# Performance work log

Measured on AMD Instinct MI355X. Metric: run time of the kernel, lower is better.

## Reference

```python
import jax, jax.numpy as jnp
import numpy as np

B = 1024      # batch
DIN = 103     # generator/encoder input dim
L1, L2 = 64, 32   # encoder layer widths (latent = 32)
E = 8         # NUM_EXPERTS
GH = 64       # gating hidden width
H = 256       # generator hidden width
DOUT = 51     # generator output dim
EPS = 1e-5    # BatchNorm eps


def setup_inputs() -> dict:
    key = jax.random.key(0)
    ks = jax.random.split(key, 24)
    s = 0.05
    f32 = jnp.float32
    return {
        "x": jax.random.normal(ks[0], (B, DIN), f32),
        # encoder Linear + BN params
        "w1": jax.random.normal(ks[1], (L1, DIN), f32) * s,
        "b1": jnp.zeros((L1,), f32),
        "gamma1": jnp.ones((L1,), f32),
        "beta1": jnp.zeros((L1,), f32),
        "w2": jax.random.normal(ks[2], (L2, L1), f32) * s,
        "b2": jnp.zeros((L2,), f32),
        "gamma2": jnp.ones((L2,), f32),
        "beta2": jnp.zeros((L2,), f32),
        # gating MLP (latent 32 -> GH -> GH -> E, ELU, softmax)
        "gw1": jax.random.normal(ks[3], (GH, L2), f32) * s,
        "gb1": jnp.zeros((GH,), f32),
        "gw2": jax.random.normal(ks[4], (GH, GH), f32) * s,
        "gb2": jnp.zeros((GH,), f32),
        "gw3": jax.random.normal(ks[5], (E, GH), f32) * s,
        "gb3": jnp.zeros((E,), f32),
        # expert weight banks for 3-layer generator (MANN style)
        "ew1": jax.random.normal(ks[6], (E, DIN, H), f32) * s,
        "eb1": jnp.zeros((E, H), f32),
        "ew2": jax.random.normal(ks[7], (E, H, H), f32) * s,
        "eb2": jnp.zeros((E, H), f32),
        "ew3": jax.random.normal(ks[8], (E, H, DOUT), f32) * s,
        "eb3": jnp.zeros((E, DOUT), f32),
    }


def _batchnorm(h, gamma, beta):
    # training-mode BatchNorm1d: per-batch mean/var (biased var, matching torch)
    m = jnp.mean(h, axis=0)
    v = jnp.mean((h - m) ** 2, axis=0)
    return gamma * (h - m) * jax.lax.rsqrt(v + EPS) + beta


def reference(x, w1, b1, gamma1, beta1, w2, b2, gamma2, beta2,
              gw1, gb1, gw2, gb2, gw3, gb3,
              ew1, eb1, ew2, eb2, ew3, eb3):
    # in-place scale of last 3 features (x[:,100:103] *= 100)
    xs = x.at[:, 100:103].multiply(100.0)
    # encoder: Linear -> BN -> ReLU, twice
    h = jax.nn.relu(_batchnorm(xs @ w1.T + b1, gamma1, beta1))
    latent = jax.nn.relu(_batchnorm(h @ w2.T + b2, gamma2, beta2))
    # gating network -> blending coefficients BC [B, E]
    g = jax.nn.elu(latent @ gw1.T + gb1)
    g = jax.nn.elu(g @ gw2.T + gb2)
    bc = jax.nn.softmax(g @ gw3.T + gb3, axis=-1)
    # MANN-style generator: per-sample expert-blended weights
    wb1 = jnp.einsum('be,eih->bih', bc, ew1)   # [B, DIN, H]
    h1 = jax.nn.elu(jnp.einsum('bi,bih->bh', xs, wb1) + bc @ eb1)
    wb2 = jnp.einsum('be,ehk->bhk', bc, ew2)   # [B, H, H]
    h2 = jax.nn.elu(jnp.einsum('bh,bhk->bk', h1, wb2) + bc @ eb2)
    wb3 = jnp.einsum('be,eho->bho', bc, ew3)   # [B, H, DOUT]
    out = jnp.einsum('bh,bho->bo', h2, wb3) + bc @ eb3
    return out
```

## Files before the change

### kernel.cpp

```cpp
#include <hip/hip_runtime.h>
#include <math.h>


#define DIN 103
#define NE  8
#define HH  256
#define DOUT 51
#define EPSBN 1e-5f

typedef __attribute__((ext_vector_type(8))) short bf16x8;
typedef __attribute__((ext_vector_type(4))) float f32x4;
typedef __attribute__((ext_vector_type(8))) unsigned short us8;
typedef unsigned short ushort_t;

__device__ __forceinline__ float eluf(float v) { return v > 0.f ? v : (expf(v) - 1.f); }
__device__ __forceinline__ unsigned short bf16h(float f) {
  unsigned u = __float_as_uint(f);
  u += 0x7FFFu + ((u >> 16) & 1u);
  return (unsigned short)(u >> 16);
}
__device__ __forceinline__ float bf16f(unsigned short h) { return __uint_as_float(((unsigned)h) << 16); }
__device__ __forceinline__ void split_bf16(float v, unsigned short& h, unsigned short& l) {
  h = bf16h(v);
  l = bf16h(v - bf16f(h));
}
#define MFMA __builtin_amdgcn_mfma_f32_16x16x32_bf16

#define O_SLOTS1 0
#define O_SLOTS2 8192
#define O_BCG    12288
#define O_H1RAW  20480
#define O_H2RAW  86016
#define O_XSH    118784
#define O_XSL    184320
#define O_W1H    249856
#define O_W1L    253952
#define O_E1H    258048
#define O_E1L    389120
#define O_E2H    520192
#define O_E2L    782336
#define O_E3H    1044480
#define O_E3L    1110016
#define O_A1H    1175552
#define O_A1L    1306624
#define O_A2H    1437696
#define O_A2L    1568768
#define O_P      1699840

__global__ __launch_bounds__(256) void k_prep(
    const float* __restrict__ x, const float* __restrict__ w1,
    const float* __restrict__ ew1, const float* __restrict__ ew2, const float* __restrict__ ew3,
    float* __restrict__ ws) {
  __shared__ float tile[32][65];
  int bk = blockIdx.x, t = threadIdx.x;
  int l2 = t & 63, c = l2 & 15, q = l2 >> 4;

  if (bk < 256) {
    int nh = bk & 3, kc = (bk >> 2) & 7, e = bk >> 5;
    int k0 = kc * 32, n0 = nh * 64;
#pragma unroll
    for (int i = 0; i < 8; ++i) {
      int kl = (t >> 6) + i * 4;
      tile[kl][t & 63] = ew2[((size_t)e * HH + k0 + kl) * HH + n0 + (t & 63)];
    }
    __syncthreads();
    int nsl = t >> 6;
    us8 H8, L8;
#pragma unroll
    for (int j = 0; j < 8; ++j) {
      unsigned short h, lo; split_bf16(tile[q * 8 + j][nsl * 16 + c], h, lo);
      H8[j] = h; L8[j] = lo;
    }
    size_t dst = (((size_t)(e * 16 + nh * 4 + nsl)) * 8 + kc) * 512 + l2 * 8;
    *(us8*)((ushort_t*)(ws + O_E2H) + dst) = H8;
    *(us8*)((ushort_t*)(ws + O_E2L) + dst) = L8;
  } else if (bk < 384) {
    int b2 = bk - 256;
    int nh = b2 & 3, kc = (b2 >> 2) & 3, e = b2 >> 4;
    int k0 = kc * 32, n0 = nh * 64;
#pragma unroll
    for (int i = 0; i < 8; ++i) {
      int kl = (t >> 6) + i * 4;
      int k = k0 + kl;
      tile[kl][t & 63] = (k < DIN) ? ew1[((size_t)e * DIN + k) * HH + n0 + (t & 63)] : 0.f;
    }
    __syncthreads();
    int nsl = t >> 6;
    us8 H8, L8;
#pragma unroll
    for (int j = 0; j < 8; ++j) {
      unsigned short h, lo; split_bf16(tile[q * 8 + j][nsl * 16 + c], h, lo);
      H8[j] = h; L8[j] = lo;
    }
    size_t dst = (((size_t)(e * 16 + nh * 4 + nsl)) * 4 + kc) * 512 + l2 * 8;
    *(us8*)((ushort_t*)(ws + O_E1H) + dst) = H8;
    *(us8*)((ushort_t*)(ws + O_E1L) + dst) = L8;
  } else if (bk < 448) {
    int b2 = bk - 384;
    int kc = b2 & 7, e = b2 >> 3;
    int k0 = kc * 32;
#pragma unroll
    for (int i = 0; i < 8; ++i) {
      int kl = (t >> 6) + i * 4;
      int n = t & 63;
      tile[kl][n] = (n < DOUT) ? ew3[((size_t)e * HH + k0 + kl) * DOUT + n] : 0.f;
    }
    __syncthreads();
    int nsl = t >> 6;
    us8 H8, L8;
#pragma unroll
    for (int j = 0; j < 8; ++j) {
      unsigned short h, lo; split_bf16(tile[q * 8 + j][nsl * 16 + c], h, lo);
      H8[j] = h; L8[j] = lo;
    }
    size_t dst = (((size_t)(e * 4 + nsl)) * 8 + kc) * 512 + l2 * 8;
    *(us8*)((ushort_t*)(ws + O_E3H) + dst) = H8;
    *(us8*)((ushort_t*)(ws + O_E3L) + dst) = L8;
  } else if (bk < 452) {
    int kc = bk - 448;
    int k0 = kc * 32;
    __shared__ float tw[64][33];
#pragma unroll
    for (int p8 = 0; p8 < 8; ++p8) {
      int j = (t >> 5) + p8 * 8;
      int kl = t & 31;
      int k = k0 + kl;
      tw[j][kl] = (k < DIN) ? w1[(size_t)j * DIN + k] : 0.f;
    }
    __syncthreads();
    int nsl = t >> 6;
    us8 H8, L8;
#pragma unroll
    for (int j = 0; j < 8; ++j) {
      unsigned short h, lo; split_bf16(tw[nsl * 16 + c][q * 8 + j], h, lo);
      H8[j] = h; L8[j] = lo;
    }
    size_t dst = ((size_t)nsl * 4 + kc) * 512 + l2 * 8;
    *(us8*)((ushort_t*)(ws + O_W1H) + dst) = H8;
    *(us8*)((ushort_t*)(ws + O_W1L) + dst) = L8;
  } else {
    int msub = bk - 452;
    __shared__ float xt[16][104];
    for (int i = t; i < 16 * 104; i += 256) {
      int b = i / 104, k = i - b * 104;
      float v = 0.f;
      if (k < DIN) { v = x[(size_t)(msub * 16 + b) * DIN + k]; if (k >= 100) v *= 100.f; }
      xt[b][k] = v;
    }
    __syncthreads();
    int kc = t >> 6;
    int m = c;
    us8 H8, L8;
#pragma unroll
    for (int j = 0; j < 8; ++j) {
      int k = kc * 32 + q * 8 + j;
      float v = (k < 104) ? xt[m][k] : 0.f;
      unsigned short h, lo; split_bf16(v, h, lo);
      H8[j] = h; L8[j] = lo;
    }
    size_t dst = ((size_t)msub * 4 + kc) * 512 + l2 * 8;
    *(us8*)((ushort_t*)(ws + O_XSH) + dst) = H8;
    *(us8*)((ushort_t*)(ws + O_XSL) + dst) = L8;
  }
}

__global__ __launch_bounds__(256) void k_enc1(const float* __restrict__ b1, float* __restrict__ ws) {
  __shared__ float tile[16][65];
  int bk = blockIdx.x, t = threadIdx.x;
  int wv = t >> 6, l = t & 63, c = l & 15, quad = l >> 4;
  const ushort_t* XsH = (const ushort_t*)(ws + O_XSH);
  const ushort_t* XsL = (const ushort_t*)(ws + O_XSL);
  const ushort_t* W1H = (const ushort_t*)(ws + O_W1H);
  const ushort_t* W1L = (const ushort_t*)(ws + O_W1L);
  float* h1raw  = ws + O_H1RAW;
  float* slots1 = ws + O_SLOTS1;
  f32x4 acc = {0.f, 0.f, 0.f, 0.f};
#pragma unroll
  for (int kc = 0; kc < 4; ++kc) {
    bf16x8 ah = *(const bf16x8*)(XsH + ((size_t)bk * 4 + kc) * 512 + l * 8);
    bf16x8 al = *(const bf16x8*)(XsL + ((size_t)bk * 4 + kc) * 512 + l * 8);
    bf16x8 bh = *(const bf16x8*)(W1H + ((size_t)wv * 4 + kc) * 512 + l * 8);
    bf16x8 bl = *(const bf16x8*)(W1L + ((size_t)wv * 4 + kc) * 512 + l * 8);
    acc = MFMA(ah, bh, acc, 0, 0, 0);
    acc = MFMA(al, bh, acc, 0, 0, 0);
    acc = MFMA(ah, bl, acc, 0, 0, 0);
  }
  int col = wv * 16 + c;
  float b1v = b1[col];
#pragma unroll
  for (int r = 0; r < 4; ++r) {
    float v = acc[r] + b1v;
    tile[quad * 4 + r][col] = v;
    h1raw[(size_t)(bk * 16 + quad * 4 + r) * 64 + col] = v;
  }
  __syncthreads();
  if (t < 64) {
    float s = 0.f, qq = 0.f;
    for (int r = 0; r < 16; ++r) { float v = tile[r][t]; s += v; qq += v * v; }
    slots1[bk * 128 + t] = s;
    slots1[bk * 128 + 64 + t] = qq;
  }
}

__global__ __launch_bounds__(256) void k_enc2(
    const float* __restrict__ gamma1, const float* __restrict__ beta1,
    const float* __restrict__ w2, const float* __restrict__ b2, float* __restrict__ ws) {
  __shared__ float w2T[64 * 33];
  __shared__ float red[128];
  __shared__ float sc1[64], sh1[64];
  __shared__ float h1b[16][64];
  __shared__ float hb2[16][32];
  float* slots1 = ws + O_SLOTS1;
  float* slots2 = ws + O_SLOTS2;
  float* h1raw  = ws + O_H1RAW;
  float* h2raw  = ws + O_H2RAW;
  int bk = blockIdx.x, t = threadIdx.x;
  int R0 = bk * 16;
  for (int i = t; i < 2048; i += 256) { int j = i >> 6, k = i & 63; w2T[k * 33 + j] = w2[i]; }
  if (t < 128) {
    float s = 0.f;
    for (int b = 0; b < 64; ++b) s += slots1[b * 128 + t];
    red[t] = s;
  }
  __syncthreads();
  if (t < 64) {
    float m = red[t] * (1.f / 1024.f);
    float v = red[64 + t] * (1.f / 1024.f) - m * m;
    float sc = gamma1[t] * rsqrtf(v + EPSBN);
    sc1[t] = sc; sh1[t] = beta1[t] - m * sc;
  }
  __syncthreads();
#pragma unroll
  for (int i = 0; i < 4; ++i) {
    int idx = t + i * 256;
    int r = idx >> 6, k = idx & 63;
    h1b[r][k] = fmaxf(fmaf(h1raw[(size_t)(R0 + r) * 64 + k], sc1[k], sh1[k]), 0.f);
  }
  __syncthreads();
#pragma unroll
  for (int i = 0; i < 2; ++i) {
    int o = t + i * 256;
    int r = o >> 5, j = o & 31;
    float acc = b2[j];
    for (int k = 0; k < 64; ++k) acc = fmaf(h1b[r][k], w2T[k * 33 + j], acc);
    hb2[r][j] = acc;
    h2raw[(size_t)(R0 + r) * 32 + j] = acc;
  }
  __syncthreads();
  if (t < 32) {
    float s = 0.f, q = 0.f;
    for (int r = 0; r < 16; ++r) { float v = hb2[r][t]; s += v; q += v * v; }
    slots2[bk * 64 + t] = s;
    slots2[bk * 64 + 32 + t] = q;
  }
}

__global__ __launch_bounds__(256) void k_gate(
    const float* __restrict__ gamma2, const float* __restrict__ beta2,
    const float* __restrict__ gw1, const float* __restrict__ gb1,
    const float* __restrict__ gw2, const float* __restrict__ gb2,
    const float* __restrict__ gw3, const float* __restrict__ gb3,
    float* __restrict__ ws) {
  __shared__ float red2[64], sc2[32], sh2[32];
  __shared__ float lat[16][32];
  __shared__ float gw1L[64 * 33], gw2L[64 * 65], gw3L[8 * 65];
  __shared__ float gb1L[64], gb2L[64], gb3L[8];
  __shared__ float g1[16][64], g2[16][64];
  float* slots2 = ws + O_SLOTS2;
  float* bcg    = ws + O_BCG;
  float* h2raw  = ws + O_H2RAW;
  int bk = blockIdx.x, t = threadIdx.x;
  int wv = t >> 6, l = t & 63;
  int R0 = bk * 16;
  for (int i = t; i < 2048; i += 256) { int j = i >> 5, k = i & 31; gw1L[j * 33 + k] = gw1[i]; }
  for (int i = t; i < 4096; i += 256) { int j = i >> 6, k = i & 63; gw2L[j * 65 + k] = gw2[i]; }
  for (int i = t; i < 512; i += 256) { int j = i >> 6, k = i & 63; gw3L[j * 65 + k] = gw3[i]; }
  if (t < 64) { gb1L[t] = gb1[t]; gb2L[t] = gb2[t]; }
  if (t < 8) gb3L[t] = gb3[t];
  if (t < 64) {
    float s = 0.f;
    for (int b = 0; b < 64; ++b) s += slots2[b * 64 + t];
    red2[t] = s;
  }
  __syncthreads();
  if (t < 32) {
    float m = red2[t] * (1.f / 1024.f);
    float v = red2[32 + t] * (1.f / 1024.f) - m * m;
    float sc = gamma2[t] * rsqrtf(v + EPSBN);
    sc2[t] = sc; sh2[t] = beta2[t] - m * sc;
  }
  __syncthreads();
#pragma unroll
  for (int i = 0; i < 2; ++i) {
    int idx = t + i * 256;
    int r = idx >> 5, cc = idx & 31;
    lat[r][cc] = fmaxf(fmaf(h2raw[(size_t)(R0 + r) * 32 + cc], sc2[cc], sh2[cc]), 0.f);
  }
  __syncthreads();
#pragma unroll
  for (int rr = 0; rr < 4; ++rr) {
    int r = wv * 4 + rr;
    float a1 = gb1L[l];
    for (int k = 0; k < 32; ++k) a1 = fmaf(gw1L[l * 33 + k], lat[r][k], a1);
    g1[r][l] = eluf(a1);
  }
  __syncthreads();
#pragma unroll
  for (int rr = 0; rr < 4; ++rr) {
    int r = wv * 4 + rr;
    float a2 = gb2L[l];
    for (int k = 0; k < 64; ++k) a2 = fmaf(gw2L[l * 65 + k], g1[r][k], a2);
    g2[r][l] = eluf(a2);
  }
  __syncthreads();
#pragma unroll
  for (int rr = 0; rr < 4; ++rr) {
    int r = wv * 4 + rr;
    if (l < 8) {
      float a3 = gb3L[l];
      for (int k = 0; k < 64; ++k) a3 = fmaf(gw3L[l * 65 + k], g2[r][k], a3);
      float mx = a3;
      mx = fmaxf(mx, __shfl_xor(mx, 1));
      mx = fmaxf(mx, __shfl_xor(mx, 2));
      mx = fmaxf(mx, __shfl_xor(mx, 4));
      float p = expf(a3 - mx);
      float sp = p;
      sp += __shfl_xor(sp, 1); sp += __shfl_xor(sp, 2); sp += __shfl_xor(sp, 4);
      bcg[(size_t)(R0 + r) * 8 + l] = p / sp;
    }
  }
}

__global__ __launch_bounds__(256) void k_gen1(float* __restrict__ ws) {
  int bk = blockIdx.x, e = blockIdx.y, t = threadIdx.x;
  int wv = t >> 6, l = t & 63, c = l & 15, quad = l >> 4;
  const ushort_t* XsH = (const ushort_t*)(ws + O_XSH);
  const ushort_t* XsL = (const ushort_t*)(ws + O_XSL);
  const ushort_t* E1H = (const ushort_t*)(ws + O_E1H);
  const ushort_t* E1L = (const ushort_t*)(ws + O_E1L);
  float* p = ws + O_P;
  f32x4 acc[4] = {};
#pragma unroll
  for (int kc = 0; kc < 4; ++kc) {
    bf16x8 ah = *(const bf16x8*)(XsH + ((size_t)bk * 4 + kc) * 512 + l * 8);
    bf16x8 al = *(const bf16x8*)(XsL + ((size_t)bk * 4 + kc) * 512 + l * 8);
#pragma unroll
    for (int nsi = 0; nsi < 4; ++nsi) {
      int ns = wv * 4 + nsi;
      size_t bo = (((size_t)(e * 16 + ns)) * 4 + kc) * 512 + l * 8;
      bf16x8 bh = *(const bf16x8*)(E1H + bo);
      bf16x8 bl = *(const bf16x8*)(E1L + bo);
      acc[nsi] = MFMA(ah, bh, acc[nsi], 0, 0, 0);
      acc[nsi] = MFMA(al, bh, acc[nsi], 0, 0, 0);
      acc[nsi] = MFMA(ah, bl, acc[nsi], 0, 0, 0);
    }
  }
  float* pe = p + (size_t)e * 262144;
#pragma unroll
  for (int nsi = 0; nsi < 4; ++nsi) {
    int col = (wv * 4 + nsi) * 16 + c;
#pragma unroll
    for (int r = 0; r < 4; ++r)
      pe[(size_t)(bk * 16 + quad * 4 + r) * 256 + col] = acc[nsi][r];
  }
}

__global__ __launch_bounds__(256) void k_gen2(float* __restrict__ ws) {
  int bk = blockIdx.x, e = blockIdx.y, t = threadIdx.x;
  int wv = t >> 6, l = t & 63, c = l & 15, quad = l >> 4;
  const ushort_t* AH = (const ushort_t*)(ws + O_A1H);
  const ushort_t* AL = (const ushort_t*)(ws + O_A1L);
  const ushort_t* E2H = (const ushort_t*)(ws + O_E2H);
  const ushort_t* E2L = (const ushort_t*)(ws + O_E2L);
  float* p = ws + O_P;
  f32x4 acc[4] = {};
#pragma unroll
  for (int kc = 0; kc < 8; ++kc) {
    bf16x8 ah = *(const bf16x8*)(AH + ((size_t)bk * 8 + kc) * 512 + l * 8);
    bf16x8 al = *(const bf16x8*)(AL + ((size_t)bk * 8 + kc) * 512 + l * 8);
#pragma unroll
    for (int nsi = 0; nsi < 4; ++nsi) {
      int ns = wv * 4 + nsi;
      size_t bo = (((size_t)(e * 16 + ns)) * 8 + kc) * 512 + l * 8;
      bf16x8 bh = *(const bf16x8*)(E2H + bo);
      bf16x8 bl = *(const bf16x8*)(E2L + bo);
      acc[nsi] = MFMA(ah, bh, acc[nsi], 0, 0, 0);
      acc[nsi] = MFMA(al, bh, acc[nsi], 0, 0, 0);
      acc[nsi] = MFMA(ah, bl, acc[nsi], 0, 0, 0);
    }
  }
  float* pe = p + (size_t)e * 262144;
#pragma unroll
  for (int nsi = 0; nsi < 4; ++nsi) {
    int col = (wv * 4 + nsi) * 16 + c;
#pragma unroll
    for (int r = 0; r < 4; ++r)
      pe[(size_t)(bk * 16 + quad * 4 + r) * 256 + col] = acc[nsi][r];
  }
}

__global__ __launch_bounds__(256) void k_gen3(float* __restrict__ ws) {
  int bk = blockIdx.x, eg = blockIdx.y, t = threadIdx.x;
  int wv = t >> 6, l = t & 63, c = l & 15, quad = l >> 4;
  int e = eg * 4 + wv;
  const ushort_t* AH = (const ushort_t*)(ws + O_A2H);
  const ushort_t* AL = (const ushort_t*)(ws + O_A2L);
  const ushort_t* E3H = (const ushort_t*)(ws + O_E3H);
  const ushort_t* E3L = (const ushort_t*)(ws + O_E3L);
  float* p3 = ws + O_P;
  f32x4 acc[4] = {};
#pragma unroll
  for (int kc = 0; kc < 8; ++kc) {
    bf16x8 ah = *(const bf16x8*)(AH + ((size_t)bk * 8 + kc) * 512 + l * 8);
    bf16x8 al = *(const bf16x8*)(AL + ((size_t)bk * 8 + kc) * 512 + l * 8);
#pragma unroll
    for (int nsi = 0; nsi < 4; ++nsi) {
      size_t bo = (((size_t)(e * 4 + nsi)) * 8 + kc) * 512 + l * 8;
      bf16x8 bh = *(const bf16x8*)(E3H + bo);
      bf16x8 bl = *(const bf16x8*)(E3L + bo);
      acc[nsi] = MFMA(ah, bh, acc[nsi], 0, 0, 0);
      acc[nsi] = MFMA(al, bh, acc[nsi], 0, 0, 0);
      acc[nsi] = MFMA(ah, bl, acc[nsi], 0, 0, 0);
    }
  }
  float* pe = p3 + (size_t)e * 65536;
#pragma unroll
  for (int nsi = 0; nsi < 4; ++nsi) {
    int col = nsi * 16 + c;
#pragma unroll
    for (int r = 0; r < 4; ++r)
      pe[(size_t)(bk * 16 + quad * 4 + r) * 64 + col] = acc[nsi][r];
  }
}

__global__ __launch_bounds__(256) void k_comb(const float* __restrict__ eb,
    float* __restrict__ ws, int dstH, int dstL) {
  int gid = blockIdx.x * 256 + threadIdx.x;
  int l2 = gid & 63, kc = (gid >> 6) & 7, msub = gid >> 9;
  int b = msub * 16 + (l2 & 15);
  int k0 = kc * 32 + (l2 >> 4) * 8;
  const float* p = ws + O_P;
  const float* bc = ws + O_BCG;
  unsigned short* ah = (unsigned short*)(ws + dstH);
  unsigned short* al = (unsigned short*)(ws + dstL);
  float wv[NE];
#pragma unroll
  for (int e = 0; e < NE; ++e) wv[e] = bc[b * NE + e];
  float s[8] = {};
#pragma unroll
  for (int e = 0; e < NE; ++e) {
    const float* pr = p + (size_t)e * 262144 + (size_t)b * HH + k0;
    float4 p0 = *(const float4*)pr, p1 = *(const float4*)(pr + 4);
    const float* er = eb + e * HH + k0;
    float4 e0 = *(const float4*)er, e1 = *(const float4*)(er + 4);
    s[0] = fmaf(wv[e], p0.x + e0.x, s[0]);
    s[1] = fmaf(wv[e], p0.y + e0.y, s[1]);
    s[2] = fmaf(wv[e], p0.z + e0.z, s[2]);
    s[3] = fmaf(wv[e], p0.w + e0.w, s[3]);
    s[4] = fmaf(wv[e], p1.x + e1.x, s[4]);
    s[5] = fmaf(wv[e], p1.y + e1.y, s[5]);
    s[6] = fmaf(wv[e], p1.z + e1.z, s[6]);
    s[7] = fmaf(wv[e], p1.w + e1.w, s[7]);
  }
  us8 H, L;
#pragma unroll
  for (int j = 0; j < 8; ++j) {
    float v = eluf(s[j]);
    unsigned short h, lo; split_bf16(v, h, lo);
    H[j] = h; L[j] = lo;
  }
  *(us8*)(ah + (size_t)gid * 8) = H;
  *(us8*)(al + (size_t)gid * 8) = L;
}

__global__ __launch_bounds__(256) void k_comb3(const float* __restrict__ eb3,
    float* __restrict__ ws, float* __restrict__ out) {
  int gid = blockIdx.x * 256 + threadIdx.x;
  int b = gid >> 6, o = gid & 63;
  if (o >= DOUT) return;
  const float* p3 = ws + O_P;
  const float* bc = ws + O_BCG;
  float s = 0.f;
#pragma unroll
  for (int e = 0; e < NE; ++e)
    s = fmaf(bc[b * NE + e], p3[(size_t)e * 65536 + (size_t)b * 64 + o] + eb3[e * DOUT + o], s);
  out[(size_t)b * DOUT + o] = s;
}

extern "C" void kernel_launch(void* const* d_in, const int* in_sizes, int n_in,
                              void* d_out, int out_size, void* d_ws, size_t ws_size,
                              hipStream_t stream) {
  const float* x      = (const float*)d_in[0];
  const float* w1     = (const float*)d_in[1];
  const float* b1     = (const float*)d_in[2];
  const float* gamma1 = (const float*)d_in[3];
  const float* beta1  = (const float*)d_in[4];
  const float* w2     = (const float*)d_in[5];
  const float* b2     = (const float*)d_in[6];
  const float* gamma2 = (const float*)d_in[7];
  const float* beta2  = (const float*)d_in[8];
  const float* gw1    = (const float*)d_in[9];
  const float* gb1    = (const float*)d_in[10];
  const float* gw2    = (const float*)d_in[11];
  const float* gb2    = (const float*)d_in[12];
  const float* gw3    = (const float*)d_in[13];
  const float* gb3    = (const float*)d_in[14];
  const float* ew1    = (const float*)d_in[15];
  const float* eb1    = (const float*)d_in[16];
  const float* ew2    = (const float*)d_in[17];
  const float* eb2    = (const float*)d_in[18];
  const float* ew3    = (const float*)d_in[19];
  const float* eb3    = (const float*)d_in[20];
  float* wsf  = (float*)d_ws;
  float* outp = (float*)d_out;

  k_prep<<<516, 256, 0, stream>>>(x, w1, ew1, ew2, ew3, wsf);
  k_enc1<<<64, 256, 0, stream>>>(b1, wsf);
  k_enc2<<<64, 256, 0, stream>>>(gamma1, beta1, w2, b2, wsf);
  k_gate<<<64, 256, 0, stream>>>(gamma2, beta2, gw1, gb1, gw2, gb2, gw3, gb3, wsf);
  k_gen1<<<dim3(64, 8), 256, 0, stream>>>(wsf);
  k_comb<<<128, 256, 0, stream>>>(eb1, wsf, O_A1H, O_A1L);
  k_gen2<<<dim3(64, 8), 256, 0, stream>>>(wsf);
  k_comb<<<128, 256, 0, stream>>>(eb2, wsf, O_A2H, O_A2L);
  k_gen3<<<dim3(64, 2), 256, 0, stream>>>(wsf);
  k_comb3<<<256, 256, 0, stream>>>(eb3, wsf, outp);
}
```

Measured before the change: 166.7 us.

## Fuse prep/enc1, gen1/gate, and expert-combine steps into gen kernels

Cuts the launch chain from ten kernels to five. Encoder layer 1 now runs as a scalar FMA matmul inside the prep kernel, and gen1 runs concurrently with the gating network in one grid. Each expert-combine step (blend + bias + ELU + bf16 split) is recomputed inside the next generator kernel through shared memory instead of a separate pass, and the final blend is done in registers in gen3. The intent is to remove launch gaps and intermediate round trips to global memory. In exchange, gen2c redoes the combine for each of the 8 experts, and gen2 and gen3 each read all 8 expert outputs.

Result: slower. 186.1 us (+11.7%).

```diff
diff --git a/kernel.cpp b/kernel.cpp
--- a/kernel.cpp
+++ b/kernel.cpp
@@ -33,25 +33,23 @@
 #define O_H2RAW  86016
 #define O_XSH    118784
 #define O_XSL    184320
-#define O_W1H    249856
-#define O_W1L    253952
-#define O_E1H    258048
-#define O_E1L    389120
-#define O_E2H    520192
-#define O_E2L    782336
-#define O_E3H    1044480
-#define O_E3L    1110016
-#define O_A1H    1175552
-#define O_A1L    1306624
-#define O_A2H    1437696
-#define O_A2L    1568768
-#define O_P      1699840
-
-__global__ __launch_bounds__(256) void k_prep(
-    const float* __restrict__ x, const float* __restrict__ w1,
+#define O_E1H    249856
+#define O_E1L    380928
+#define O_E2H    512000
+#define O_E2L    774144
+#define O_E3H    1036288
+#define O_E3L    1101824
+#define O_P      1167360
+#define O_P2     3264512
+
+__global__ __launch_bounds__(256) void k_prep_enc1(
+    const float* __restrict__ x, const float* __restrict__ w1, const float* __restrict__ b1,
     const float* __restrict__ ew1, const float* __restrict__ ew2, const float* __restrict__ ew3,
     float* __restrict__ ws) {
   __shared__ float tile[32][65];
+  __shared__ float w1L[64 * DIN];
+  __shared__ float xr16[16][104];
+  __shared__ float hb[16][64];
   int bk = blockIdx.x, t = threadIdx.x;
   int l2 = t & 63, c = l2 & 15, q = l2 >> 4;
 
@@ -116,89 +114,56 @@
     size_t dst = (((size_t)(e * 4 + nsl)) * 8 + kc) * 512 + l2 * 8;
     *(us8*)((ushort_t*)(ws + O_E3H) + dst) = H8;
     *(us8*)((ushort_t*)(ws + O_E3L) + dst) = L8;
-  } else if (bk < 452) {
-    int kc = bk - 448;
-    int k0 = kc * 32;
-    __shared__ float tw[64][33];
-#pragma unroll
-    for (int p8 = 0; p8 < 8; ++p8) {
-      int j = (t >> 5) + p8 * 8;
-      int kl = t & 31;
-      int k = k0 + kl;
-      tw[j][kl] = (k < DIN) ? w1[(size_t)j * DIN + k] : 0.f;
-    }
-    __syncthreads();
-    int nsl = t >> 6;
-    us8 H8, L8;
-#pragma unroll
-    for (int j = 0; j < 8; ++j) {
-      unsigned short h, lo; split_bf16(tw[nsl * 16 + c][q * 8 + j], h, lo);
-      H8[j] = h; L8[j] = lo;
-    }
-    size_t dst = ((size_t)nsl * 4 + kc) * 512 + l2 * 8;
-    *(us8*)((ushort_t*)(ws + O_W1H) + dst) = H8;
-    *(us8*)((ushort_t*)(ws + O_W1L) + dst) = L8;
-  } else {
-    int msub = bk - 452;
-    __shared__ float xt[16][104];
+  } else if (bk < 512) {
+    int msub = bk - 448;
     for (int i = t; i < 16 * 104; i += 256) {
       int b = i / 104, k = i - b * 104;
       float v = 0.f;
       if (k < DIN) { v = x[(size_t)(msub * 16 + b) * DIN + k]; if (k >= 100) v *= 100.f; }
-      xt[b][k] = v;
+      xr16[b][k] = v;
     }
     __syncthreads();
     int kc = t >> 6;
-    int m = c;
     us8 H8, L8;
 #pragma unroll
     for (int j = 0; j < 8; ++j) {
       int k = kc * 32 + q * 8 + j;
-      float v = (k < 104) ? xt[m][k] : 0.f;
+      float v = (k < 104) ? xr16[c][k] : 0.f;
       unsigned short h, lo; split_bf16(v, h, lo);
       H8[j] = h; L8[j] = lo;
     }
     size_t dst = ((size_t)msub * 4 + kc) * 512 + l2 * 8;
     *(us8*)((ushort_t*)(ws + O_XSH) + dst) = H8;
     *(us8*)((ushort_t*)(ws + O_XSL) + dst) = L8;
-  }
-}
-
-__global__ __launch_bounds__(256) void k_enc1(const float* __restrict__ b1, float* __restrict__ ws) {
-  __shared__ float tile[16][65];
-  int bk = blockIdx.x, t = threadIdx.x;
-  int wv = t >> 6, l = t & 63, c = l & 15, quad = l >> 4;
-  const ushort_t* XsH = (const ushort_t*)(ws + O_XSH);
-  const ushort_t* XsL = (const ushort_t*)(ws + O_XSL);
-  const ushort_t* W1H = (const ushort_t*)(ws + O_W1H);
-  const ushort_t* W1L = (const ushort_t*)(ws + O_W1L);
-  float* h1raw  = ws + O_H1RAW;
-  float* slots1 = ws + O_SLOTS1;
-  f32x4 acc = {0.f, 0.f, 0.f, 0.f};
-#pragma unroll
-  for (int kc = 0; kc < 4; ++kc) {
-    bf16x8 ah = *(const bf16x8*)(XsH + ((size_t)bk * 4 + kc) * 512 + l * 8);
-    bf16x8 al = *(const bf16x8*)(XsL + ((size_t)bk * 4 + kc) * 512 + l * 8);
-    bf16x8 bh = *(const bf16x8*)(W1H + ((size_t)wv * 4 + kc) * 512 + l * 8);
-    bf16x8 bl = *(const bf16x8*)(W1L + ((size_t)wv * 4 + kc) * 512 + l * 8);
-    acc = MFMA(ah, bh, acc, 0, 0, 0);
-    acc = MFMA(al, bh, acc, 0, 0, 0);
-    acc = MFMA(ah, bl, acc, 0, 0, 0);
-  }
-  int col = wv * 16 + c;
-  float b1v = b1[col];
-#pragma unroll
-  for (int r = 0; r < 4; ++r) {
-    float v = acc[r] + b1v;
-    tile[quad * 4 + r][col] = v;
-    h1raw[(size_t)(bk * 16 + quad * 4 + r) * 64 + col] = v;
-  }
-  __syncthreads();
-  if (t < 64) {
-    float s = 0.f, qq = 0.f;
-    for (int r = 0; r < 16; ++r) { float v = tile[r][t]; s += v; qq += v * v; }
-    slots1[bk * 128 + t] = s;
-    slots1[bk * 128 + 64 + t] = qq;
+  } else {
+    float* slots1 = ws + O_SLOTS1;
+    float* h1raw  = ws + O_H1RAW;
+    int bkl = bk - 512;
+    int r0 = bkl * 16;
+    for (int i = t; i < 64 * DIN; i += 256) w1L[i] = w1[i];
+    for (int i = t; i < 16 * 104; i += 256) {
+      int r = i / 104, c2 = i - r * 104;
+      float v = 0.f;
+      if (c2 < DIN) { v = x[(size_t)(r0 + r) * DIN + c2]; if (c2 >= 100) v *= 100.f; }
+      xr16[r][c2] = v;
+    }
+    __syncthreads();
+#pragma unroll
+    for (int i = 0; i < 4; ++i) {
+      int idx = t + i * 256;
+      int r = idx >> 6, j = idx & 63;
+      float acc = b1[j];
+      for (int k = 0; k < DIN; ++k) acc = fmaf(xr16[r][k], w1L[j * DIN + k], acc);
+      hb[r][j] = acc;
+      h1raw[(size_t)(r0 + r) * 64 + j] = acc;
+    }
+    __syncthreads();
+    if (t < 64) {
+      float s = 0.f, qq = 0.f;
+      for (int r = 0; r < 16; ++r) { float v = hb[r][t]; s += v; qq += v * v; }
+      slots1[bkl * 128 + t] = s;
+      slots1[bkl * 128 + 64 + t] = qq;
+    }
   }
 }
 
@@ -255,141 +220,182 @@
   }
 }
 
-__global__ __launch_bounds__(256) void k_gate(
+__global__ __launch_bounds__(256) void k_gen1_gate(
     const float* __restrict__ gamma2, const float* __restrict__ beta2,
     const float* __restrict__ gw1, const float* __restrict__ gb1,
     const float* __restrict__ gw2, const float* __restrict__ gb2,
     const float* __restrict__ gw3, const float* __restrict__ gb3,
     float* __restrict__ ws) {
-  __shared__ float red2[64], sc2[32], sh2[32];
-  __shared__ float lat[16][32];
-  __shared__ float gw1L[64 * 33], gw2L[64 * 65], gw3L[8 * 65];
-  __shared__ float gb1L[64], gb2L[64], gb3L[8];
-  __shared__ float g1[16][64], g2[16][64];
-  float* slots2 = ws + O_SLOTS2;
-  float* bcg    = ws + O_BCG;
-  float* h2raw  = ws + O_H2RAW;
-  int bk = blockIdx.x, t = threadIdx.x;
+  int blk = blockIdx.x, t = threadIdx.x;
   int wv = t >> 6, l = t & 63;
+  if (blk < 512) {
+    int bk = blk >> 3, e = blk & 7;
+    int c = l & 15, quad = l >> 4;
+    const ushort_t* XsH = (const ushort_t*)(ws + O_XSH);
+    const ushort_t* XsL = (const ushort_t*)(ws + O_XSL);
+    const ushort_t* E1H = (const ushort_t*)(ws + O_E1H);
+    const ushort_t* E1L = (const ushort_t*)(ws + O_E1L);
+    float* p = ws + O_P;
+    f32x4 acc[4] = {};
+#pragma unroll
+    for (int kc = 0; kc < 4; ++kc) {
+      bf16x8 ah = *(const bf16x8*)(XsH + ((size_t)bk * 4 + kc) * 512 + l * 8);
+      bf16x8 al = *(const bf16x8*)(XsL + ((size_t)bk * 4 + kc) * 512 + l * 8);
+#pragma unroll
+      for (int nsi = 0; nsi < 4; ++nsi) {
+        int ns = wv * 4 + nsi;
+        size_t bo = (((size_t)(e * 16 + ns)) * 4 + kc) * 512 + l * 8;
+        bf16x8 bh = *(const bf16x8*)(E1H + bo);
+        bf16x8 bl = *(const bf16x8*)(E1L + bo);
+        acc[nsi] = MFMA(ah, bh, acc[nsi], 0, 0, 0);
+        acc[nsi] = MFMA(al, bh, acc[nsi], 0, 0, 0);
+        acc[nsi] = MFMA(ah, bl, acc[nsi], 0, 0, 0);
+      }
+    }
+    float* pe = p + (size_t)e * 262144;
+#pragma unroll
+    for (int nsi = 0; nsi < 4; ++nsi) {
+      int col = (wv * 4 + nsi) * 16 + c;
+#pragma unroll
+      for (int r = 0; r < 4; ++r)
+        pe[(size_t)(bk * 16 + quad * 4 + r) * 256 + col] = acc[nsi][r];
+    }
+  } else {
+    __shared__ float red2[64], sc2[32], sh2[32];
+    __shared__ float lat[16][32];
+    __shared__ float gw1L[64 * 33], gw2L[64 * 65], gw3L[8 * 65];
+    __shared__ float gb1L[64], gb2L[64], gb3L[8];
+    __shared__ float g1[16][64], g2[16][64];
+    float* slots2 = ws + O_SLOTS2;
+    float* bcg    = ws + O_BCG;
+    float* h2raw  = ws + O_H2RAW;
+    int bk = blk - 512;
+    int R0 = bk * 16;
+    for (int i = t; i < 2048; i += 256) { int j = i >> 5, k = i & 31; gw1L[j * 33 + k] = gw1[i]; }
+    for (int i = t; i < 4096; i += 256) { int j = i >> 6, k = i & 63; gw2L[j * 65 + k] = gw2[i]; }
+    for (int i = t; i < 512; i += 256) { int j = i >> 6, k = i & 63; gw3L[j * 65 + k] = gw3[i]; }
+    if (t < 64) { gb1L[t] = gb1[t]; gb2L[t] = gb2[t]; }
+    if (t < 8) gb3L[t] = gb3[t];
+    if (t < 64) {
+      float s = 0.f;
+      for (int b = 0; b < 64; ++b) s += slots2[b * 64 + t];
+      red2[t] = s;
+    }
+    __syncthreads();
+    if (t < 32) {
+      float m = red2[t] * (1.f / 1024.f);
+      float v = red2[32 + t] * (1.f / 1024.f) - m * m;
+      float sc = gamma2[t] * rsqrtf(v + EPSBN);
+      sc2[t] = sc; sh2[t] = beta2[t] - m * sc;
+    }
+    __syncthreads();
+#pragma unroll
+    for (int i = 0; i < 2; ++i) {
+      int idx = t + i * 256;
+      int r = idx >> 5, cc = idx & 31;
+      lat[r][cc] = fmaxf(fmaf(h2raw[(size_t)(R0 + r) * 32 + cc], sc2[cc], sh2[cc]), 0.f);
+    }
+    __syncthreads();
+#pragma unroll
+    for (int rr = 0; rr < 4; ++rr) {
+      int r = wv * 4 + rr;
+      float a1 = gb1L[l];
+      for (int k = 0; k < 32; ++k) a1 = fmaf(gw1L[l * 33 + k], lat[r][k], a1);
+      g1[r][l] = eluf(a1);
+    }
+    __syncthreads();
+#pragma unroll
+    for (int rr = 0; rr < 4; ++rr) {
+      int r = wv * 4 + rr;
+      float a2 = gb2L[l];
+      for (int k = 0; k < 64; ++k) a2 = fmaf(gw2L[l * 65 + k], g1[r][k], a2);
+      g2[r][l] = eluf(a2);
+    }
+    __syncthreads();
+#pragma unroll
+    for (int rr = 0; rr < 4; ++rr) {
+      int r = wv * 4 + rr;
+      if (l < 8) {
+        float a3 = gb3L[l];
+        for (int k = 0; k < 64; ++k) a3 = fmaf(gw3L[l * 65 + k], g2[r][k], a3);
+        float mx = a3;
+        mx = fmaxf(mx, __shfl_xor(mx, 1));
+        mx = fmaxf(mx, __shfl_xor(mx, 2));
+        mx = fmaxf(mx, __shfl_xor(mx, 4));
+        float p = expf(a3 - mx);
+        float sp = p;
+        sp += __shfl_xor(sp, 1); sp += __shfl_xor(sp, 2); sp += __shfl_xor(sp, 4);
+        bcg[(size_t)(R0 + r) * 8 + l] = p / sp;
+      }
+    }
+  }
+}
+
+__global__ __launch_bounds__(256) void k_gen2c(const float* __restrict__ eb1, float* __restrict__ ws) {
+  __shared__ __attribute__((aligned(16))) unsigned short aHs[4096], aLs[4096];
+  int bk = blockIdx.x, e = blockIdx.y, t = threadIdx.x;
+  int wv = t >> 6, l = t & 63, c = l & 15, quad = l >> 4;
   int R0 = bk * 16;
-  for (int i = t; i < 2048; i += 256) { int j = i >> 5, k = i & 31; gw1L[j * 33 + k] = gw1[i]; }
-  for (int i = t; i < 4096; i += 256) { int j = i >> 6, k = i & 63; gw2L[j * 65 + k] = gw2[i]; }
-  for (int i = t; i < 512; i += 256) { int j = i >> 6, k = i & 63; gw3L[j * 65 + k] = gw3[i]; }
-  if (t < 64) { gb1L[t] = gb1[t]; gb2L[t] = gb2[t]; }
-  if (t < 8) gb3L[t] = gb3[t];
-  if (t < 64) {
-    float s = 0.f;
-    for (int b = 0; b < 64; ++b) s += slots2[b * 64 + t];
-    red2[t] = s;
-  }
-  __syncthreads();
-  if (t < 32) {
-    float m = red2[t] * (1.f / 1024.f);
-    float v = red2[32 + t] * (1.f / 1024.f) - m * m;
-    float sc = gamma2[t] * rsqrtf(v + EPSBN);
-    sc2[t] = sc; sh2[t] = beta2[t] - m * sc;
-  }
-  __syncthreads();
+  const float* P   = ws + O_P;
+  const float* bcg = ws + O_BCG;
+  const ushort_t* E2H = (const ushort_t*)(ws + O_E2H);
+  const ushort_t* E2L = (const ushort_t*)(ws + O_E2L);
+  float* P2 = ws + O_P2;
 #pragma unroll
   for (int i = 0; i < 2; ++i) {
     int idx = t + i * 256;
-    int r = idx >> 5, cc = idx & 31;
-    lat[r][cc] = fmaxf(fmaf(h2raw[(size_t)(R0 + r) * 32 + cc], sc2[cc], sh2[cc]), 0.f);
-  }
-  __syncthreads();
-#pragma unroll
-  for (int rr = 0; rr < 4; ++rr) {
-    int r = wv * 4 + rr;
-    float a1 = gb1L[l];
-    for (int k = 0; k < 32; ++k) a1 = fmaf(gw1L[l * 33 + k], lat[r][k], a1);
-    g1[r][l] = eluf(a1);
-  }
-  __syncthreads();
-#pragma unroll
-  for (int rr = 0; rr < 4; ++rr) {
-    int r = wv * 4 + rr;
-    float a2 = gb2L[l];
-    for (int k = 0; k < 64; ++k) a2 = fmaf(gw2L[l * 65 + k], g1[r][k], a2);
-    g2[r][l] = eluf(a2);
-  }
-  __syncthreads();
-#pragma unroll
-  for (int rr = 0; rr < 4; ++rr) {
-    int r = wv * 4 + rr;
-    if (l < 8) {
-      float a3 = gb3L[l];
-      for (int k = 0; k < 64; ++k) a3 = fmaf(gw3L[l * 65 + k], g2[r][k], a3);
-      float mx = a3;
-      mx = fmaxf(mx, __shfl_xor(mx, 1));
-      mx = fmaxf(mx, __shfl_xor(mx, 2));
-      mx = fmaxf(mx, __shfl_xor(mx, 4));
-      float p = expf(a3 - mx);
-      float sp = p;
-      sp += __shfl_xor(sp, 1); sp += __shfl_xor(sp, 2); sp += __shfl_xor(sp, 4);
-      bcg[(size_t)(R0 + r) * 8 + l] = p / sp;
-    }
-  }
-}
-
-__global__ __launch_bounds__(256) void k_gen1(float* __restrict__ ws) {
-  int bk = blockIdx.x, e = blockIdx.y, t = threadIdx.x;
-  int wv = t >> 6, l = t & 63, c = l & 15, quad = l >> 4;
-  const ushort_t* XsH = (const ushort_t*)(ws + O_XSH);
-  const ushort_t* XsL = (const ushort_t*)(ws + O_XSL);
-  const ushort_t* E1H = (const ushort_t*)(ws + O_E1H);
-  const ushort_t* E1L = (const ushort_t*)(ws + O_E1L);
-  float* p = ws + O_P;
+    int kc = idx >> 6, l2 = idx & 63;
+    int b = R0 + (l2 & 15);
+    int k0 = kc * 32 + (l2 >> 4) * 8;
+    float s[8] = {};
+#pragma unroll
+    for (int e2 = 0; e2 < 8; ++e2) {
+      float w8 = bcg[b * 8 + e2];
+      const float* pr = P + (size_t)e2 * 262144 + (size_t)b * 256 + k0;
+      float4 p0 = *(const float4*)pr, p1 = *(const float4*)(pr + 4);
+      const float* er = eb1 + e2 * 256 + k0;
+      float4 e0 = *(const float4*)er, e1 = *(const float4*)(er + 4);
+      s[0] = fmaf(w8, p0.x + e0.x, s[0]);
+      s[1] = fmaf(w8, p0.y + e0.y, s[1]);
+      s[2] = fmaf(w8, p0.z + e0.z, s[2]);
+      s[3] = fmaf(w8, p0.w + e0.w, s[3]);
+      s[4] = fmaf(w8, p1.x + e1.x, s[4]);
+      s[5] = fmaf(w8, p1.y + e1.y, s[5]);
+      s[6] = fmaf(w8, p1.z + e1.z, s[6]);
+      s[7] = fmaf(w8, p1.w + e1.w, s[7]);
+    }
+    us8 H, L;
+#pragma unroll
+    for (int j = 0; j < 8; ++j) {
+      float v = eluf(s[j]);
+      unsigned short h, lo; split_bf16(v, h, lo);
+      H[j] = h; L[j] = lo;
+    }
+    *(us8*)(aHs + idx * 8) = H;
+    *(us8*)(aLs + idx * 8) = L;
+  }
+  __syncthreads();
+  bf16x8 ah[8], al[8];
+#pragma unroll
+  for (int kc = 0; kc < 8; ++kc) {
+    ah[kc] = *(const bf16x8*)(aHs + kc * 512 + l * 8);
+    al[kc] = *(const bf16x8*)(aLs + kc * 512 + l * 8);
+  }
   f32x4 acc[4] = {};
 #pragma unroll
-  for (int kc = 0; kc < 4; ++kc) {
-    bf16x8 ah = *(const bf16x8*)(XsH + ((size_t)bk * 4 + kc) * 512 + l * 8);
-    bf16x8 al = *(const bf16x8*)(XsL + ((size_t)bk * 4 + kc) * 512 + l * 8);
-#pragma unroll
-    for (int nsi = 0; nsi < 4; ++nsi) {
-      int ns = wv * 4 + nsi;
-      size_t bo = (((size_t)(e * 16 + ns)) * 4 + kc) * 512 + l * 8;
-      bf16x8 bh = *(const bf16x8*)(E1H + bo);
-      bf16x8 bl = *(const bf16x8*)(E1L + bo);
-      acc[nsi] = MFMA(ah, bh, acc[nsi], 0, 0, 0);
-      acc[nsi] = MFMA(al, bh, acc[nsi], 0, 0, 0);
-      acc[nsi] = MFMA(ah, bl, acc[nsi], 0, 0, 0);
-    }
-  }
-  float* pe = p + (size_t)e * 262144;
-#pragma unroll
-  for (int nsi = 0; nsi < 4; ++nsi) {
-    int col = (wv * 4 + nsi) * 16 + c;
-#pragma unroll
-    for (int r = 0; r < 4; ++r)
-      pe[(size_t)(bk * 16 + quad * 4 + r) * 256 + col] = acc[nsi][r];
-  }
-}
-
-__global__ __launch_bounds__(256) void k_gen2(float* __restrict__ ws) {
-  int bk = blockIdx.x, e = blockIdx.y, t = threadIdx.x;
-  int wv = t >> 6, l = t & 63, c = l & 15, quad = l >> 4;
-  const ushort_t* AH = (const ushort_t*)(ws + O_A1H);
-  const ushort_t* AL = (const ushort_t*)(ws + O_A1L);
-  const ushort_t* E2H = (const ushort_t*)(ws + O_E2H);
-  const ushort_t* E2L = (const ushort_t*)(ws + O_E2L);
-  float* p = ws + O_P;
-  f32x4 acc[4] = {};
-#pragma unroll
   for (int kc = 0; kc < 8; ++kc) {
-    bf16x8 ah = *(const bf16x8*)(AH + ((size_t)bk * 8 + kc) * 512 + l * 8);
-    bf16x8 al = *(const bf16x8*)(AL + ((size_t)bk * 8 + kc) * 512 + l * 8);
 #pragma unroll
     for (int nsi = 0; nsi < 4; ++nsi) {
       int ns = wv * 4 + nsi;
       size_t bo = (((size_t)(e * 16 + ns)) * 8 + kc) * 512 + l * 8;
       bf16x8 bh = *(const bf16x8*)(E2H + bo);
       bf16x8 bl = *(const bf16x8*)(E2L + bo);
-      acc[nsi] = MFMA(ah, bh, acc[nsi], 0, 0, 0);
-      acc[nsi] = MFMA(al, bh, acc[nsi], 0, 0, 0);
-      acc[nsi] = MFMA(ah, bl, acc[nsi], 0, 0, 0);
-    }
-  }
-  float* pe = p + (size_t)e * 262144;
+      acc[nsi] = MFMA(ah[kc], bh, acc[nsi], 0, 0, 0);
+      acc[nsi] = MFMA(al[kc], bh, acc[nsi], 0, 0, 0);
+      acc[nsi] = MFMA(ah[kc], bl, acc[nsi], 0, 0, 0);
+    }
+  }
+  float* pe = P2 + (size_t)e * 262144;
 #pragma unroll
   for (int nsi = 0; nsi < 4; ++nsi) {
     int col = (wv * 4 + nsi) * 16 + c;
@@ -399,92 +405,101 @@
   }
 }
 
-__global__ __launch_bounds__(256) void k_gen3(float* __restrict__ ws) {
-  int bk = blockIdx.x, eg = blockIdx.y, t = threadIdx.x;
+__global__ __launch_bounds__(256) void k_gen3c(const float* __restrict__ eb2,
+    const float* __restrict__ eb3, float* __restrict__ ws, float* __restrict__ out) {
+  __shared__ __attribute__((aligned(16))) unsigned short aHs[4096], aLs[4096];
+  __shared__ float bcL[16][8];
+  __shared__ float eb3L[8][64];
+  __shared__ float p3s[4][16][64];
+  int bk = blockIdx.x, t = threadIdx.x;
   int wv = t >> 6, l = t & 63, c = l & 15, quad = l >> 4;
-  int e = eg * 4 + wv;
-  const ushort_t* AH = (const ushort_t*)(ws + O_A2H);
-  const ushort_t* AL = (const ushort_t*)(ws + O_A2L);
+  int R0 = bk * 16;
+  const float* P2  = ws + O_P2;
+  const float* bcg = ws + O_BCG;
   const ushort_t* E3H = (const ushort_t*)(ws + O_E3H);
   const ushort_t* E3L = (const ushort_t*)(ws + O_E3L);
-  float* p3 = ws + O_P;
-  f32x4 acc[4] = {};
+  if (t < 128) bcL[t >> 3][t & 7] = bcg[(size_t)(R0 + (t >> 3)) * 8 + (t & 7)];
+  for (int i = t; i < 512; i += 256) {
+    int e = i >> 6, n = i & 63;
+    eb3L[e][n] = (n < DOUT) ? eb3[e * DOUT + n] : 0.f;
+  }
+#pragma unroll
+  for (int i = 0; i < 2; ++i) {
+    int idx = t + i * 256;
+    int kc = idx >> 6, l2 = idx & 63;
+    int b = R0 + (l2 & 15);
+    int k0 = kc * 32 + (l2 >> 4) * 8;
+    float s[8] = {};
+#pragma unroll
+    for (int e2 = 0; e2 < 8; ++e2) {
+      float w8 = bcg[b * 8 + e2];
+      const float* pr = P2 + (size_t)e2 * 262144 + (size_t)b * 256 + k0;
+      float4 p0 = *(const float4*)pr, p1 = *(const float4*)(pr + 4);
+      const float* er = eb2 + e2 * 256 + k0;
+      float4 e0 = *(const float4*)er, e1 = *(const float4*)(er + 4);
+      s[0] = fmaf(w8, p0.x + e0.x, s[0]);
+      s[1] = fmaf(w8, p0.y + e0.y, s[1]);
+      s[2] = fmaf(w8, p0.z + e0.z, s[2]);
+      s[3] = fmaf(w8, p0.w + e0.w, s[3]);
+      s[4] = fmaf(w8, p1.x + e1.x, s[4]);
+      s[5] = fmaf(w8, p1.y + e1.y, s[5]);
+      s[6] = fmaf(w8, p1.z + e1.z, s[6]);
+      s[7] = fmaf(w8, p1.w + e1.w, s[7]);
+    }
+    us8 H, L;
+#pragma unroll
+    for (int j = 0; j < 8; ++j) {
+      float v = eluf(s[j]);
+      unsigned short h, lo; split_bf16(v, h, lo);
+      H[j] = h; L[j] = lo;
+    }
+    *(us8*)(aHs + idx * 8) = H;
+    *(us8*)(aLs + idx * 8) = L;
+  }
+  __syncthreads();
+  bf16x8 ah[8], al[8];
 #pragma unroll
   for (int kc = 0; kc < 8; ++kc) {
-    bf16x8 ah = *(const bf16x8*)(AH + ((size_t)bk * 8 + kc) * 512 + l * 8);
-    bf16x8 al = *(const bf16x8*)(AL + ((size_t)bk * 8 + kc) * 512 + l * 8);
+    ah[kc] = *(const bf16x8*)(aHs + kc * 512 + l * 8);
+    al[kc] = *(const bf16x8*)(aLs + kc * 512 + l * 8);
+  }
+  f32x4 tot[4] = {};
+#pragma unroll
+  for (int ei = 0; ei < 2; ++ei) {
+    int e = wv * 2 + ei;
 #pragma unroll
     for (int nsi = 0; nsi < 4; ++nsi) {
-      size_t bo = (((size_t)(e * 4 + nsi)) * 8 + kc) * 512 + l * 8;
-      bf16x8 bh = *(const bf16x8*)(E3H + bo);
-      bf16x8 bl = *(const bf16x8*)(E3L + bo);
-      acc[nsi] = MFMA(ah, bh, acc[nsi], 0, 0, 0);
-      acc[nsi] = MFMA(al, bh, acc[nsi], 0, 0, 0);
-      acc[nsi] = MFMA(ah, bl, acc[nsi], 0, 0, 0);
-    }
-  }
-  float* pe = p3 + (size_t)e * 65536;
-#pragma unroll
-  for (int nsi = 0; nsi < 4; ++nsi) {
-    int col = nsi * 16 + c;
+      f32x4 acc = {0.f, 0.f, 0.f, 0.f};
+#pragma unroll
+      for (int kc = 0; kc < 8; ++kc) {
+        size_t bo = (((size_t)(e * 4 + nsi)) * 8 + kc) * 512 + l * 8;
+        bf16x8 bh = *(const bf16x8*)(E3H + bo);
+        bf16x8 bl = *(const bf16x8*)(E3L + bo);
+        acc = MFMA(ah[kc], bh, acc, 0, 0, 0);
+        acc = MFMA(al[kc], bh, acc, 0, 0, 0);
+        acc = MFMA(ah[kc], bl, acc, 0, 0, 0);
+      }
+#pragma unroll
+      for (int r = 0; r < 4; ++r)
+        tot[nsi][r] = fmaf(bcL[quad * 4 + r][e], acc[r], tot[nsi][r]);
+    }
+  }
+#pragma unroll
+  for (int nsi = 0; nsi < 4; ++nsi)
 #pragma unroll
     for (int r = 0; r < 4; ++r)
-      pe[(size_t)(bk * 16 + quad * 4 + r) * 64 + col] = acc[nsi][r];
-  }
-}
-
-__global__ __launch_bounds__(256) void k_comb(const float* __restrict__ eb,
-    float* __restrict__ ws, int dstH, int dstL) {
-  int gid = blockIdx.x * 256 + threadIdx.x;
-  int l2 = gid & 63, kc = (gid >> 6) & 7, msub = gid >> 9;
-  int b = msub * 16 + (l2 & 15);
-  int k0 = kc * 32 + (l2 >> 4) * 8;
-  const float* p = ws + O_P;
-  const float* bc = ws + O_BCG;
-  unsigned short* ah = (unsigned short*)(ws + dstH);
-  unsigned short* al = (unsigned short*)(ws + dstL);
-  float wv[NE];
-#pragma unroll
-  for (int e = 0; e < NE; ++e) wv[e] = bc[b * NE + e];
-  float s[8] = {};
-#pragma unroll
-  for (int e = 0; e < NE; ++e) {
-    const float* pr = p + (size_t)e * 262144 + (size_t)b * HH + k0;
-    float4 p0 = *(const float4*)pr, p1 = *(const float4*)(pr + 4);
-    const float* er = eb + e * HH + k0;
-    float4 e0 = *(const float4*)er, e1 = *(const float4*)(er + 4);
-    s[0] = fmaf(wv[e], p0.x + e0.x, s[0]);
-    s[1] = fmaf(wv[e], p0.y + e0.y, s[1]);
-    s[2] = fmaf(wv[e], p0.z + e0.z, s[2]);
-    s[3] = fmaf(wv[e], p0.w + e0.w, s[3]);
-    s[4] = fmaf(wv[e], p1.x + e1.x, s[4]);
-    s[5] = fmaf(wv[e], p1.y + e1.y, s[5]);
-    s[6] = fmaf(wv[e], p1.z + e1.z, s[6]);
-    s[7] = fmaf(wv[e], p1.w + e1.w, s[7]);
-  }
-  us8 H, L;
-#pragma unroll
-  for (int j = 0; j < 8; ++j) {
-    float v = eluf(s[j]);
-    unsigned short h, lo; split_bf16(v, h, lo);
-    H[j] = h; L[j] = lo;
-  }
-  *(us8*)(ah + (size_t)gid * 8) = H;
-  *(us8*)(al + (size_t)gid * 8) = L;
-}
-
-__global__ __launch_bounds__(256) void k_comb3(const float* __restrict__ eb3,
-    float* __restrict__ ws, float* __restrict__ out) {
-  int gid = blockIdx.x * 256 + threadIdx.x;
-  int b = gid >> 6, o = gid & 63;
-  if (o >= DOUT) return;
-  const float* p3 = ws + O_P;
-  const float* bc = ws + O_BCG;
-  float s = 0.f;
-#pragma unroll
-  for (int e = 0; e < NE; ++e)
-    s = fmaf(bc[b * NE + e], p3[(size_t)e * 65536 + (size_t)b * 64 + o] + eb3[e * DOUT + o], s);
-  out[(size_t)b * DOUT + o] = s;
+      p3s[wv][quad * 4 + r][nsi * 16 + c] = tot[nsi][r];
+  __syncthreads();
+#pragma unroll
+  for (int i = 0; i < 4; ++i) {
+    int idx = t + i * 256;
+    int row = idx >> 6, col = idx & 63;
+    float s = p3s[0][row][col] + p3s[1][row][col] + p3s[2][row][col] + p3s[3][row][col];
+    float bb = 0.f;
+#pragma unroll
+    for (int e = 0; e < 8; ++e) bb = fmaf(bcL[row][e], eb3L[e][col], bb);
+    if (col < DOUT) out[(size_t)(R0 + row) * DOUT + col] = s + bb;
+  }
 }
 
 extern "C" void kernel_launch(void* const* d_in, const int* in_sizes, int n_in,
@@ -514,14 +529,9 @@
   float* wsf  = (float*)d_ws;
   float* outp = (float*)d_out;
 
-  k_prep<<<516, 256, 0, stream>>>(x, w1, ew1, ew2, ew3, wsf);
-  k_enc1<<<64, 256, 0, stream>>>(b1, wsf);
+  k_prep_enc1<<<576, 256, 0, stream>>>(x, w1, b1, ew1, ew2, ew3, wsf);
   k_enc2<<<64, 256, 0, stream>>>(gamma1, beta1, w2, b2, wsf);
-  k_gate<<<64, 256, 0, stream>>>(gamma2, beta2, gw1, gb1, gw2, gb2, gw3, gb3, wsf);
-  k_gen1<<<dim3(64, 8), 256, 0, stream>>>(wsf);
-  k_comb<<<128, 256, 0, stream>>>(eb1, wsf, O_A1H, O_A1L);
-  k_gen2<<<dim3(64, 8), 256, 0, stream>>>(wsf);
-  k_comb<<<128, 256, 0, stream>>>(eb2, wsf, O_A2H, O_A2L);
-  k_gen3<<<dim3(64, 2), 256, 0, stream>>>(wsf);
-  k_comb3<<<256, 256, 0, stream>>>(eb3, wsf, outp);
-}
+  k_gen1_gate<<<576, 256, 0, stream>>>(gamma2, beta2, gw1, gb1, gw2, gb2, gw3, gb3, wsf);
+  k_gen2c<<<dim3(64, 8), 256, 0, stream>>>(eb1, wsf);
+  k_gen3c<<<64, 256, 0, stream>>>(eb2, eb3, wsf, outp);
+}
```
